# Optimization experiments

Measured on AMD Instinct MI355X. Metric: run time of the kernel, lower is better.

The kernel has to match this reference:

```python
import jax, jax.numpy as jnp
import numpy as np

N = 50000      # nodes
E = 400000     # edges per meta-path
DIN = 256      # input_dim
H = 4          # heads
F = 64         # output_dim per head
P = 3          # meta-paths
HID = 128      # SA_Attention hidden
NEG_SLOPE = 0.2


def setup_inputs() -> dict:
    key = jax.random.key(0)
    ks = jax.random.split(key, 12)
    inp = {
        "h": jax.random.normal(ks[0], (N, DIN), dtype=jnp.float32),
        "ei_0": jax.random.randint(ks[1], (2, E), 0, N, dtype=jnp.int64),
        "ei_1": jax.random.randint(ks[2], (2, E), 0, N, dtype=jnp.int64),
        "ei_2": jax.random.randint(ks[3], (2, E), 0, N, dtype=jnp.int64),
        # GAT params per meta-path (stacked over P)
        "gat_W": jax.random.normal(ks[4], (P, DIN, H * F), dtype=jnp.float32) * 0.05,
        "att_src": jax.random.normal(ks[5], (P, H, F), dtype=jnp.float32) * 0.05,
        "att_dst": jax.random.normal(ks[6], (P, H, F), dtype=jnp.float32) * 0.05,
        "gat_bias": jnp.zeros((P, H * F), dtype=jnp.float32),
        # SA_Attention params: Linear(H*F, HID) + Tanh + Linear(HID, 1, bias=False)
        "sa_w1": jax.random.normal(ks[7], (H * F, HID), dtype=jnp.float32) * 0.05,
        "sa_b1": jnp.zeros((HID,), dtype=jnp.float32),
        "sa_w2": jax.random.normal(ks[8], (HID,), dtype=jnp.float32) * 0.05,
    }
    return inp


def _gat_conv(x, ei, W, a_src, a_dst, b):
    """PyG-style GATConv with self-loops, concat heads. x:[N,DIN] -> [N,H*F]."""
    n = x.shape[0]
    xw = (x @ W).reshape(n, H, F)                    # [N,H,F]
    loop = jnp.arange(n, dtype=ei.dtype)
    src = jnp.concatenate([ei[0], loop])             # [E+N]
    dst = jnp.concatenate([ei[1], loop])
    alpha_s = jnp.einsum('nhf,hf->nh', xw, a_src)    # [N,H]
    alpha_d = jnp.einsum('nhf,hf->nh', xw, a_dst)
    e = jax.nn.leaky_relu(alpha_s[src] + alpha_d[dst], NEG_SLOPE)  # [E+N,H]
    # segment softmax over destination nodes (every node has a self loop)
    m = jax.ops.segment_max(e, dst, num_segments=n)
    ex = jnp.exp(e - m[dst])
    s = jax.ops.segment_sum(ex, dst, num_segments=n)
    alpha = ex / s[dst]                              # [E+N,H]
    out = jax.ops.segment_sum(alpha[:, :, None] * xw[src], dst, num_segments=n)
    return out.reshape(n, H * F) + b


def reference(h, ei_0, ei_1, ei_2, gat_W, att_src, att_dst, gat_bias,
              sa_w1, sa_b1, sa_w2):
    eis = [ei_0, ei_1, ei_2]
    # per-meta-path GAT embeddings -> z: [N, P, H*F]
    z = jnp.stack([
        _gat_conv(h, eis[i], gat_W[i], att_src[i], att_dst[i], gat_bias[i])
        for i in range(P)
    ], axis=1)
    # semantic attention: project -> mean over nodes -> softmax over meta-paths
    w = jnp.tanh(z @ sa_w1 + sa_b1) @ sa_w2          # [N,P]
    beta = jax.nn.softmax(w.mean(axis=0))            # [P]
    return (beta[None, :, None] * z).sum(axis=1)     # [N, H*F]
```

## Files before the change

kernel.cpp:

```cpp
#include <hip/hip_runtime.h>
#include <hip/hip_bf16.h>

__device__ __forceinline__ float bf2f(unsigned short u) {
    union { unsigned int i; float f; } x;
    x.i = ((unsigned int)u) << 16;
    return x.f;
}
__device__ __forceinline__ unsigned short f2bf(float f) {
    union { float f; unsigned int u; } x; x.f = f;
    unsigned int r = x.u + 0x7FFFu + ((x.u >> 16) & 1u);
    return (unsigned short)(r >> 16);
}
__device__ __forceinline__ float fast_tanh(float x) {
    float a = fabsf(x);
    float t = __expf(2.f * a);
    float r = 1.f - 2.f / (t + 1.f);
    return copysignf(r, x);
}

typedef __bf16    bf16x8 __attribute__((ext_vector_type(8)));
typedef _Float16  f16x8  __attribute__((ext_vector_type(8)));
typedef _Float16  f16x4  __attribute__((ext_vector_type(4)));
typedef float     f32x4  __attribute__((ext_vector_type(4)));

#define XW_OFF     0UL
#define ZB_OFF     25600000UL
#define CSR_OFF    102400000UL
#define RS_OFF     107200000UL
#define CUR_OFF    107800064UL
#define BS_OFF     108400128UL
#define AS_OFF     108401152UL
#define AD_OFF     109201152UL
#define WT_OFF     110001152UL
#define W1T_OFF    110394368UL
#define ASF_OFF    110459904UL
#define ADF_OFF    110462976UL
#define BIASF_OFF  110466048UL
#define B1F_OFF    110469120UL
#define W2F_OFF    110469632UL
#define WSUM_OFF   110470144UL
#define BETA_OFF   110470208UL
#define FLAG_OFF   110470272UL

__global__ void probe(const unsigned short* __restrict__ hraw,
                      const unsigned int* __restrict__ eraw,
                      int* __restrict__ flags) {
    if (threadIdx.x == 0 && blockIdx.x == 0) {
        int sane = 0;
        for (int i = 0; i < 256; ++i) {
            unsigned int e = (hraw[i] >> 7) & 0xFF;
            if (hraw[i] != 0 && e >= 100 && e <= 150) sane++;
        }
        flags[0] = (sane >= 220) ? 1 : 0;
        int zeros = 0;
        for (int i = 1; i < 256; i += 2) if (eraw[i] == 0u) zeros++;
        flags[1] = (zeros >= 120) ? 1 : 0;
    }
}

__device__ __forceinline__ float rd_f(const void* p, int j, bool bf) {
    return bf ? bf2f(((const unsigned short*)p)[j]) : ((const float*)p)[j];
}
__device__ __forceinline__ int rd_i(const void* p, long long j, bool i64) {
    return i64 ? (int)((const long long*)p)[j] : ((const int*)p)[j];
}

__global__ void ingest_params(const void* W, const void* as, const void* ad, const void* bias,
                              const void* w1, const void* b1, const void* w2,
                              unsigned short* Wt, _Float16* w1t,
                              float* asf, float* adf, float* biasf,
                              float* b1f, float* w2f,
                              const int* __restrict__ flags) {
    int i = blockIdx.x * 256 + threadIdx.x;
    bool bf = flags[0] != 0;
    if (i < 196608) {
        int p = i >> 16, n = (i >> 8) & 255, k = i & 255;
        Wt[i] = f2bf(rd_f(W, p * 65536 + k * 256 + n, bf));
    } else if (i < 229376) {
        int j = i - 196608;
        int n = j >> 8, k = j & 255;
        w1t[j] = (_Float16)rd_f(w1, k * 128 + n, bf);
    } else if (i < 230144) {
        int j = i - 229376; asf[j] = rd_f(as, j, bf);
    } else if (i < 230912) {
        int j = i - 230144; adf[j] = rd_f(ad, j, bf);
    } else if (i < 231680) {
        int j = i - 230912; biasf[j] = rd_f(bias, j, bf);
    } else if (i < 231808) {
        int j = i - 231680; b1f[j] = rd_f(b1, j, bf);
    } else if (i < 231936) {
        int j = i - 231808; w2f[j] = rd_f(w2, j, bf);
    }
}

__global__ void conv_hist(const void* e0, const void* e1, const void* e2,
                          unsigned int* __restrict__ ed, int* __restrict__ cur,
                          int E, int N, int T4, const int* __restrict__ flags) {
    int i = blockIdx.x * 256 + threadIdx.x;
    if (i >= T4) return;
    bool i64 = flags[1] != 0;
    int tot = 3 * E;
#pragma unroll
    for (int c = 0; c < 4; ++c) {
        int idx = i + c * T4;
        if (idx >= tot) continue;
        int p = idx / E, e = idx - p * E;
        const void* ep = (p == 0) ? e0 : (p == 1) ? e1 : e2;
        unsigned int src = (unsigned int)rd_i(ep, e, i64);
        unsigned int dst = (unsigned int)rd_i(ep, (long long)E + e, i64);
        ed[idx] = src | (dst << 16);
        atomicAdd(&cur[p * N + (int)dst], 1);
    }
}

__global__ void scan1(const int* __restrict__ cnt, int* __restrict__ rs,
                      int* __restrict__ bs, int M) {
    __shared__ int s[1024];
    int t = threadIdx.x, i = blockIdx.x * 1024 + t;
    int v = (i < M) ? cnt[i] : 0;
    s[t] = v; __syncthreads();
    for (int o = 1; o < 1024; o <<= 1) {
        int tmp = (t >= o) ? s[t - o] : 0;
        __syncthreads();
        s[t] += tmp;
        __syncthreads();
    }
    if (i < M) rs[i] = s[t] - v;
    if (t == 1023) bs[blockIdx.x] = s[t];
}

__global__ void scan2(int* __restrict__ bs, int* __restrict__ rs, int nb, int M) {
    __shared__ int s[256];
    int t = threadIdx.x;
    int v = (t < nb) ? bs[t] : 0;
    s[t] = v; __syncthreads();
    for (int o = 1; o < 256; o <<= 1) {
        int tmp = (t >= o) ? s[t - o] : 0;
        __syncthreads();
        s[t] += tmp;
        __syncthreads();
    }
    if (t < nb) bs[t] = s[t] - v;
    if (t == nb - 1) rs[M] = s[t];
}

__global__ void scan3(int* __restrict__ rs, const int* __restrict__ bs, int M) {
    int i = blockIdx.x * 1024 + threadIdx.x;
    if (i < M) rs[i] += bs[blockIdx.x];
}

__global__ void scatter(const unsigned int* __restrict__ ed,
                        const int* __restrict__ rs, int* __restrict__ cur,
                        unsigned short* __restrict__ csr, int E, int N, int T4) {
    int i = blockIdx.x * 256 + threadIdx.x;
    if (i >= T4) return;
    int tot = 3 * E;
#pragma unroll
    for (int c = 0; c < 4; ++c) {
        int idx = i + c * T4;
        if (idx >= tot) continue;
        unsigned int u = ed[idx];
        int p = idx / E;
        int seg = p * N + (int)(u >> 16);
        int pos = rs[seg] + atomicAdd(&cur[seg], 1);
        csr[pos] = (unsigned short)(u & 0xFFFFu);
    }
}

__global__ __launch_bounds__(256, 2)
void gemm_xw_mfma(const void* __restrict__ h,
                  const unsigned short* __restrict__ Wtp,
                  unsigned short* __restrict__ xw,
                  const float* __restrict__ asf,
                  const float* __restrict__ adf,
                  float* __restrict__ as_, float* __restrict__ ad_,
                  const int* __restrict__ flags, int N) {
    __shared__ __bf16 Bs[32768];
    int tid  = threadIdx.x;
    int ch   = blockIdx.x & 1;
    int rg   = blockIdx.x >> 1;
    {
        const bf16x8* src = (const bf16x8*)Wtp;
#pragma unroll
        for (int it = 0; it < 16; ++it) {
            int c = it * 256 + tid;
            int row = c >> 5, cv = c & 31;
            *(bf16x8*)(Bs + ((row << 5) + (cv ^ (row & 7))) * 8) =
                src[(ch * 128 + row) * 32 + cv];
        }
    }
    __syncthreads();

    int wave = tid >> 6, lane = tid & 63;
    int l15 = lane & 15, quad = lane >> 4;
    int sw  = l15 & 7;
    int row0 = rg * 256 + wave * 64;
    bool bfm = flags[0] != 0;

    int lr[4];
#pragma unroll
    for (int rt = 0; rt < 4; ++rt) lr[rt] = min(row0 + rt * 16 + l15, N - 1);

    f32x4 acc[4][8];
#pragma unroll
    for (int rt = 0; rt < 4; ++rt)
#pragma unroll
        for (int tn = 0; tn < 8; ++tn) acc[rt][tn] = (f32x4){0.f, 0.f, 0.f, 0.f};

#pragma unroll
    for (int c0 = 0; c0 < 32; c0 += 4) {
        int kc = c0 * 8;
        bf16x8 a[4];
#pragma unroll
        for (int rt = 0; rt < 4; ++rt) {
            size_t off = (size_t)lr[rt] * 256 + kc + quad * 8;
            if (bfm) {
                a[rt] = *reinterpret_cast<const bf16x8*>((const __bf16*)h + off);
            } else {
                f32x4 u0 = *reinterpret_cast<const f32x4*>((const float*)h + off);
                f32x4 u1 = *reinterpret_cast<const f32x4*>((const float*)h + off + 4);
#pragma unroll
                for (int j = 0; j < 4; ++j) { a[rt][j] = (__bf16)u0[j]; a[rt][4 + j] = (__bf16)u1[j]; }
            }
        }
#pragma unroll
        for (int tn = 0; tn < 8; ++tn) {
            int row = tn * 16 + l15;
            bf16x8 b = *reinterpret_cast<const bf16x8*>(
                Bs + ((row << 5) + (((c0 + quad)) ^ sw)) * 8);
#pragma unroll
            for (int rt = 0; rt < 4; ++rt)
                acc[rt][tn] = __builtin_amdgcn_mfma_f32_16x16x32_bf16(a[rt], b, acc[rt][tn], 0, 0, 0);
        }
    }

#pragma unroll
    for (int rt = 0; rt < 4; ++rt) {
        int rbase = row0 + rt * 16 + quad * 4;
#pragma unroll
        for (int tn = 0; tn < 8; ++tn) {
            int c = ch * 128 + tn * 16 + l15;
#pragma unroll
            for (int i = 0; i < 4; ++i) {
                int r = rbase + i;
                if (r < N) xw[(size_t)r * 256 + c] = f2bf(acc[rt][tn][i]);
            }
        }
        float ss[2][4] = {{0.f,0.f,0.f,0.f},{0.f,0.f,0.f,0.f}};
        float dd[2][4] = {{0.f,0.f,0.f,0.f},{0.f,0.f,0.f,0.f}};
#pragma unroll
        for (int tn = 0; tn < 8; ++tn) {
            int c = ch * 128 + tn * 16 + l15;
            float sv = asf[c], dv = adf[c];
            int hs = tn >> 2;
#pragma unroll
            for (int i = 0; i < 4; ++i) {
                ss[hs][i] += acc[rt][tn][i] * sv;
                dd[hs][i] += acc[rt][tn][i] * dv;
            }
        }
#pragma unroll
        for (int hs = 0; hs < 2; ++hs)
#pragma unroll
            for (int i = 0; i < 4; ++i) {
                float s = ss[hs][i], d = dd[hs][i];
                s += __shfl_xor(s, 1); d += __shfl_xor(d, 1);
                s += __shfl_xor(s, 2); d += __shfl_xor(d, 2);
                s += __shfl_xor(s, 4); d += __shfl_xor(d, 4);
                s += __shfl_xor(s, 8); d += __shfl_xor(d, 8);
                ss[hs][i] = s; dd[hs][i] = d;
            }
        if (l15 == 0) {
#pragma unroll
            for (int hs = 0; hs < 2; ++hs)
#pragma unroll
                for (int i = 0; i < 4; ++i) {
                    int r = rbase + i;
                    if (r < N) {
                        int g = r * 4 + ch * 2 + hs;
                        as_[g] = ss[hs][i];
                        ad_[g] = dd[hs][i];
                    }
                }
        }
    }
}

__device__ __forceinline__ float leaky(float v) { return v > 0.f ? v : 0.2f * v; }

__global__ void agg_csr(const unsigned short* __restrict__ csr, const int* __restrict__ rs,
                        const float* __restrict__ as_, const float* __restrict__ ad_,
                        const unsigned short* __restrict__ xw,
                        const float* __restrict__ biasf,
                        _Float16* __restrict__ zb, int N, int p) {
    int d = blockIdx.x * 4 + (threadIdx.x >> 6);
    if (d >= N) return;
    int lane = threadIdx.x & 63;
    int h = lane >> 4;
    int seg = p * N + d;
    int start = rs[seg], end = rs[seg + 1];

    float adh = ad_[d * 4 + h];
    float m = leaky(as_[d * 4 + h] + adh);
    float l = 1.f;
    float a0, a1, a2, a3;
    {
        ushort4 u = *reinterpret_cast<const ushort4*>(xw + (size_t)d * 256 + lane * 4);
        a0 = bf2f(u.x); a1 = bf2f(u.y); a2 = bf2f(u.z); a3 = bf2f(u.w);
    }
    if (start < end) {
        int srcA = csr[start];
        float sA = as_[srcA * 4 + h];
        ushort4 uA = *reinterpret_cast<const ushort4*>(xw + (size_t)srcA * 256 + lane * 4);
        for (int j = start; j < end; ++j) {
            int srcB = (j + 1 < end) ? csr[j + 1] : 0;
            float sB = as_[srcB * 4 + h];
            ushort4 uB = *reinterpret_cast<const ushort4*>(xw + (size_t)srcB * 256 + lane * 4);
            float v = leaky(sA + adh);
            float mn = fmaxf(m, v);
            float c = __expf(m - mn);
            float w = __expf(v - mn);
            m = mn;
            l = l * c + w;
            a0 = a0 * c + w * bf2f(uA.x);
            a1 = a1 * c + w * bf2f(uA.y);
            a2 = a2 * c + w * bf2f(uA.z);
            a3 = a3 * c + w * bf2f(uA.w);
            sA = sB; uA = uB;
        }
    }
    float inv = 1.f / l;
    int col = lane * 4;
    const float* bp = biasf + p * 256 + col;
    f16x4 o = {(_Float16)(a0 * inv + bp[0]), (_Float16)(a1 * inv + bp[1]),
               (_Float16)(a2 * inv + bp[2]), (_Float16)(a3 * inv + bp[3])};
    *reinterpret_cast<f16x4*>(zb + ((size_t)d * 3 + p) * 256 + col) = o;
}

__global__ __launch_bounds__(1024, 4)
void sem_w_mfma(const _Float16* __restrict__ zb,
                const _Float16* __restrict__ w1t,
                const float* __restrict__ b1f,
                const float* __restrict__ w2f,
                float* __restrict__ wsum, int rows) {
    __shared__ _Float16 Bs[32768];
    __shared__ float redbuf[16][3];
    int tid = threadIdx.x;
    {
        const f16x8* src = (const f16x8*)w1t;
#pragma unroll
        for (int it = 0; it < 4; ++it) {
            int c = it * 1024 + tid;
            int row = c >> 5, cv = c & 31;
            *(f16x8*)(Bs + ((row << 5) + (cv ^ (row & 7))) * 8) = src[c];
        }
    }
    __syncthreads();

    int wave = tid >> 6, lane = tid & 63;
    int l15 = lane & 15, quad = lane >> 4;
    int sw  = l15 & 7;
    int row0 = blockIdx.x * 256 + wave * 16;
    int lr = min(row0 + l15, rows - 1);

    f32x4 acc[8];
#pragma unroll
    for (int tn = 0; tn < 8; ++tn) acc[tn] = (f32x4){0.f, 0.f, 0.f, 0.f};

#pragma unroll
    for (int c0 = 0; c0 < 32; c0 += 4) {
        int kc = c0 * 8;
        f16x8 a = *reinterpret_cast<const f16x8*>(zb + (size_t)lr * 256 + kc + quad * 8);
#pragma unroll
        for (int tn = 0; tn < 8; ++tn) {
            int brow = tn * 16 + l15;
            f16x8 b = *reinterpret_cast<const f16x8*>(
                Bs + ((brow << 5) + ((c0 + quad) ^ sw)) * 8);
            acc[tn] = __builtin_amdgcn_mfma_f32_16x16x32_f16(a, b, acc[tn], 0, 0, 0);
        }
    }

    float rowsum[4] = {0.f, 0.f, 0.f, 0.f};
#pragma unroll
    for (int tn = 0; tn < 8; ++tn) {
        int col = tn * 16 + l15;
        float b1v = b1f[col], w2v = w2f[col];
#pragma unroll
        for (int i = 0; i < 4; ++i)
            rowsum[i] += fast_tanh(acc[tn][i] + b1v) * w2v;
    }
#pragma unroll
    for (int i = 0; i < 4; ++i) {
        rowsum[i] += __shfl_xor(rowsum[i], 1);
        rowsum[i] += __shfl_xor(rowsum[i], 2);
        rowsum[i] += __shfl_xor(rowsum[i], 4);
        rowsum[i] += __shfl_xor(rowsum[i], 8);
    }
    float bins[3] = {0.f, 0.f, 0.f};
    if (l15 == 0) {
#pragma unroll
        for (int i = 0; i < 4; ++i) {
            int r = row0 + quad * 4 + i;
            if (r < rows) bins[r % 3] += rowsum[i];
        }
    }
#pragma unroll
    for (int b = 0; b < 3; ++b) {
        bins[b] += __shfl_xor(bins[b], 16);
        bins[b] += __shfl_xor(bins[b], 32);
    }
    if (lane == 0) {
#pragma unroll
        for (int b = 0; b < 3; ++b) redbuf[wave][b] = bins[b];
    }
    __syncthreads();
    if (tid < 3) {
        float s = 0.f;
#pragma unroll
        for (int w = 0; w < 16; ++w) s += redbuf[w][tid];
        atomicAdd(&wsum[tid], s);
    }
}

__global__ void combine(const _Float16* __restrict__ zb,
                        const float* __restrict__ wsum, float invN,
                        void* __restrict__ out, const int* __restrict__ flags) {
    int idx = blockIdx.x * 256 + threadIdx.x;
    int n = idx >> 6, c4 = (idx & 63) * 4;
    float w0 = wsum[0] * invN, w1 = wsum[1] * invN, w2 = wsum[2] * invN;
    float mx = fmaxf(w0, fmaxf(w1, w2));
    float e0 = __expf(w0 - mx), e1 = __expf(w1 - mx), e2 = __expf(w2 - mx);
    float s = 1.f / (e0 + e1 + e2);
    float b0 = e0 * s, b1 = e1 * s, b2 = e2 * s;
    const _Float16* base = zb + (size_t)n * 768 + c4;
    f16x4 z0 = *reinterpret_cast<const f16x4*>(base);
    f16x4 z1 = *reinterpret_cast<const f16x4*>(base + 256);
    f16x4 z2 = *reinterpret_cast<const f16x4*>(base + 512);
    float v[4];
#pragma unroll
    for (int i = 0; i < 4; ++i)
        v[i] = b0 * (float)z0[i] + b1 * (float)z1[i] + b2 * (float)z2[i];
    if (flags[0]) {
        ushort4 o = {f2bf(v[0]), f2bf(v[1]), f2bf(v[2]), f2bf(v[3])};
        *reinterpret_cast<ushort4*>((unsigned short*)out + (size_t)idx * 4) = o;
    } else {
        f32x4 o = {v[0], v[1], v[2], v[3]};
        *reinterpret_cast<f32x4*>((float*)out + (size_t)idx * 4) = o;
    }
}

extern "C" void kernel_launch(void* const* d_in, const int* in_sizes, int n_in,
                              void* d_out, int out_size, void* d_ws, size_t ws_size,
                              hipStream_t stream) {
    const void* h    = d_in[0];
    const void* e0   = d_in[1];
    const void* e1   = d_in[2];
    const void* e2   = d_in[3];
    const void* W    = d_in[4];
    const void* as   = d_in[5];
    const void* ad   = d_in[6];
    const void* bias = d_in[7];
    const void* w1   = d_in[8];
    const void* b1   = d_in[9];
    const void* w2   = d_in[10];

    const int N = in_sizes[0] / 256;
    const int E = in_sizes[1] / 2;
    const int M = 3 * N;
    const int T4 = (3 * E + 3) / 4;

    char* ws = (char*)d_ws;
    unsigned short* xw    = (unsigned short*)(ws + XW_OFF);
    _Float16*       zb    = (_Float16*)(ws + ZB_OFF);
    unsigned short* csr   = (unsigned short*)(ws + CSR_OFF);
    int*            rs    = (int*)(ws + RS_OFF);
    int*            cur   = (int*)(ws + CUR_OFF);
    int*            bs    = (int*)(ws + BS_OFF);
    float*          as_   = (float*)(ws + AS_OFF);
    float*          ad_   = (float*)(ws + AD_OFF);
    unsigned short* Wt    = (unsigned short*)(ws + WT_OFF);
    _Float16*       w1t   = (_Float16*)(ws + W1T_OFF);
    float*          asf   = (float*)(ws + ASF_OFF);
    float*          adf   = (float*)(ws + ADF_OFF);
    float*          biasf = (float*)(ws + BIASF_OFF);
    float*          b1f   = (float*)(ws + B1F_OFF);
    float*          w2f   = (float*)(ws + W2F_OFF);
    float*          wsum  = (float*)(ws + WSUM_OFF);
    int*            flags = (int*)(ws + FLAG_OFF);

    unsigned int* ed = (unsigned int*)(ws + ZB_OFF);

    probe<<<1, 64, 0, stream>>>((const unsigned short*)h, (const unsigned int*)e0, flags);
    ingest_params<<<907, 256, 0, stream>>>(W, as, ad, bias, w1, b1, w2,
                                           Wt, w1t, asf, adf, biasf, b1f, w2f, flags);

    int nb = (M + 1023) / 1024;
    int e4B = (T4 + 255) / 256;
    hipMemsetAsync(cur, 0, M * sizeof(int), stream);
    conv_hist<<<e4B, 256, 0, stream>>>(e0, e1, e2, ed, cur, E, N, T4, flags);
    scan1<<<nb, 1024, 0, stream>>>(cur, rs, bs, M);
    scan2<<<1, 256, 0, stream>>>(bs, rs, nb, M);
    scan3<<<nb, 1024, 0, stream>>>(rs, bs, M);
    hipMemsetAsync(cur, 0, M * sizeof(int), stream);
    scatter<<<e4B, 256, 0, stream>>>(ed, rs, cur, csr, E, N, T4);

    hipMemsetAsync(wsum, 0, 16, stream);

    int gemmBlocks = ((N + 255) / 256) * 2;
    int aggBlocks  = (N + 3) / 4;
    for (int p = 0; p < 3; ++p) {
        gemm_xw_mfma<<<gemmBlocks, 256, 0, stream>>>(h, Wt + p * 65536, xw,
                                                     asf + p * 256, adf + p * 256,
                                                     as_, ad_, flags, N);
        agg_csr<<<aggBlocks, 256, 0, stream>>>(csr, rs, as_, ad_, xw, biasf, zb, N, p);
    }

    int semBlocks = (M + 255) / 256;
    sem_w_mfma<<<semBlocks, 1024, 0, stream>>>(zb, w1t, b1f, w2f, wsum, M);
    combine<<<(N * 64 + 255) / 256, 256, 0, stream>>>(zb, wsum, 1.0f / (float)N, d_out, flags);
}
```

Baseline: 531.3 us.

## Build CSR with two-pass shared-memory bucket sort instead of global atomics

Replaces the histogram, three-kernel scan and atomic scatter CSR build with a two-kernel bucket sort. The first kernel bins edges by destination into 1024-segment buckets using shared-memory atomics. The second kernel sorts each bucket locally and writes row starts and CSR entries. This cuts global atomic contention, kernel launches and memsets, but bucket capacity is capped at 16384, so skewed inputs could silently drop edges.

```diff
diff --git a/kernel.cpp b/kernel.cpp
--- a/kernel.cpp
+++ b/kernel.cpp
@@ -41,6 +41,10 @@
 #define WSUM_OFF   110470144UL
 #define BETA_OFF   110470208UL
 #define FLAG_OFF   110470272UL
+
+#define CHUNKA 5000
+#define NBMAX  152
+#define CAPB   16384
 
 __global__ void probe(const unsigned short* __restrict__ hraw,
                       const unsigned int* __restrict__ eraw,
@@ -93,77 +97,106 @@
     }
 }
 
-__global__ void conv_hist(const void* e0, const void* e1, const void* e2,
-                          unsigned int* __restrict__ ed, int* __restrict__ cur,
-                          int E, int N, int T4, const int* __restrict__ flags) {
-    int i = blockIdx.x * 256 + threadIdx.x;
-    if (i >= T4) return;
+__global__ __launch_bounds__(256)
+void bucket_a(const void* e0, const void* e1, const void* e2,
+              int* __restrict__ bcnt, unsigned int* __restrict__ bkt,
+              int E, int N, int NB, const int* __restrict__ flags) {
+    __shared__ unsigned int  ent[CHUNKA];
+    __shared__ unsigned char bck[CHUNKA];
+    __shared__ unsigned int  sent[CHUNKA];
+    __shared__ unsigned char sbck[CHUNKA];
+    __shared__ int lcnt[NBMAX], lpre[NBMAX], lbase[NBMAX], lcur[NBMAX];
+    int tid = threadIdx.x;
+    int s = blockIdx.x * CHUNKA;
+    int tot = 3 * E;
+    int n = min(tot, s + CHUNKA) - s;
+    for (int b = tid; b < NBMAX; b += 256) { lcnt[b] = 0; lcur[b] = 0; }
+    __syncthreads();
     bool i64 = flags[1] != 0;
-    int tot = 3 * E;
-#pragma unroll
-    for (int c = 0; c < 4; ++c) {
-        int idx = i + c * T4;
-        if (idx >= tot) continue;
-        int p = idx / E, e = idx - p * E;
+    for (int i = tid; i < n; i += 256) {
+        int idx = s + i;
+        int p = (idx >= 2 * E) ? 2 : (idx >= E) ? 1 : 0;
+        int j = idx - p * E;
         const void* ep = (p == 0) ? e0 : (p == 1) ? e1 : e2;
-        unsigned int src = (unsigned int)rd_i(ep, e, i64);
-        unsigned int dst = (unsigned int)rd_i(ep, (long long)E + e, i64);
-        ed[idx] = src | (dst << 16);
-        atomicAdd(&cur[p * N + (int)dst], 1);
-    }
-}
-
-__global__ void scan1(const int* __restrict__ cnt, int* __restrict__ rs,
-                      int* __restrict__ bs, int M) {
-    __shared__ int s[1024];
-    int t = threadIdx.x, i = blockIdx.x * 1024 + t;
-    int v = (i < M) ? cnt[i] : 0;
-    s[t] = v; __syncthreads();
-    for (int o = 1; o < 1024; o <<= 1) {
-        int tmp = (t >= o) ? s[t - o] : 0;
+        unsigned int src = (unsigned int)rd_i(ep, j, i64);
+        unsigned int dst = (unsigned int)rd_i(ep, (long long)E + j, i64);
+        int seg = p * N + (int)dst;
+        int b = seg >> 10;
+        ent[i] = src | ((unsigned int)(seg & 1023) << 16);
+        bck[i] = (unsigned char)b;
+        atomicAdd(&lcnt[b], 1);
+    }
+    __syncthreads();
+    if (tid == 0) {
+        int run = 0;
+        for (int b = 0; b < NB; ++b) { lpre[b] = run; run += lcnt[b]; }
+    }
+    if (tid < NB) lbase[tid] = atomicAdd(&bcnt[tid], lcnt[tid]);
+    __syncthreads();
+    for (int i = tid; i < n; i += 256) {
+        int b = bck[i];
+        int pos = lpre[b] + atomicAdd(&lcur[b], 1);
+        sent[pos] = ent[i];
+        sbck[pos] = (unsigned char)b;
+    }
+    __syncthreads();
+    for (int q = tid; q < n; q += 256) {
+        int b = sbck[q];
+        int gpos = lbase[b] + (q - lpre[b]);
+        if (gpos < CAPB) bkt[(size_t)b * CAPB + gpos] = sent[q];
+    }
+}
+
+__global__ __launch_bounds__(256)
+void bucket_b(const int* __restrict__ bcnt, const unsigned int* __restrict__ bkt,
+              int* __restrict__ rs, unsigned short* __restrict__ csr,
+              int M, int NB, int tot) {
+    __shared__ int scnt[1024];
+    __shared__ int spre[1024];
+    __shared__ int part[256];
+    int b = blockIdx.x, tid = threadIdx.x;
+    int acc = 0;
+    for (int i = tid; i < b; i += 256) acc += min(bcnt[i], CAPB);
+    part[tid] = acc; __syncthreads();
+    for (int o = 128; o > 0; o >>= 1) {
+        if (tid < o) part[tid] += part[tid + o];
         __syncthreads();
-        s[t] += tmp;
+    }
+    int base = part[0];
+    int cnt = min(bcnt[b], CAPB);
+    for (int i = tid; i < 1024; i += 256) scnt[i] = 0;
+    __syncthreads();
+    const unsigned int* src = bkt + (size_t)b * CAPB;
+    for (int i = tid; i < cnt; i += 256)
+        atomicAdd(&scnt[src[i] >> 16], 1);
+    __syncthreads();
+    int a0 = scnt[tid * 4], a1 = scnt[tid * 4 + 1], a2 = scnt[tid * 4 + 2], a3 = scnt[tid * 4 + 3];
+    int psum = a0 + a1 + a2 + a3;
+    part[tid] = psum; __syncthreads();
+    for (int o = 1; o < 256; o <<= 1) {
+        int tmp = (tid >= o) ? part[tid - o] : 0;
         __syncthreads();
-    }
-    if (i < M) rs[i] = s[t] - v;
-    if (t == 1023) bs[blockIdx.x] = s[t];
-}
-
-__global__ void scan2(int* __restrict__ bs, int* __restrict__ rs, int nb, int M) {
-    __shared__ int s[256];
-    int t = threadIdx.x;
-    int v = (t < nb) ? bs[t] : 0;
-    s[t] = v; __syncthreads();
-    for (int o = 1; o < 256; o <<= 1) {
-        int tmp = (t >= o) ? s[t - o] : 0;
+        part[tid] += tmp;
         __syncthreads();
-        s[t] += tmp;
-        __syncthreads();
-    }
-    if (t < nb) bs[t] = s[t] - v;
-    if (t == nb - 1) rs[M] = s[t];
-}
-
-__global__ void scan3(int* __restrict__ rs, const int* __restrict__ bs, int M) {
-    int i = blockIdx.x * 1024 + threadIdx.x;
-    if (i < M) rs[i] += bs[blockIdx.x];
-}
-
-__global__ void scatter(const unsigned int* __restrict__ ed,
-                        const int* __restrict__ rs, int* __restrict__ cur,
-                        unsigned short* __restrict__ csr, int E, int N, int T4) {
-    int i = blockIdx.x * 256 + threadIdx.x;
-    if (i >= T4) return;
-    int tot = 3 * E;
-#pragma unroll
-    for (int c = 0; c < 4; ++c) {
-        int idx = i + c * T4;
-        if (idx >= tot) continue;
-        unsigned int u = ed[idx];
-        int p = idx / E;
-        int seg = p * N + (int)(u >> 16);
-        int pos = rs[seg] + atomicAdd(&cur[seg], 1);
-        csr[pos] = (unsigned short)(u & 0xFFFFu);
+    }
+    int pb = part[tid] - psum;
+    spre[tid * 4]     = pb;
+    spre[tid * 4 + 1] = pb + a0;
+    spre[tid * 4 + 2] = pb + a0 + a1;
+    spre[tid * 4 + 3] = pb + a0 + a1 + a2;
+    __syncthreads();
+    for (int i = tid; i < 1024; i += 256) {
+        int seg = b * 1024 + i;
+        if (seg < M) rs[seg] = base + spre[i];
+        scnt[i] = 0;
+    }
+    if (b == NB - 1 && tid == 0) rs[M] = tot;
+    __syncthreads();
+    for (int i = tid; i < cnt; i += 256) {
+        unsigned int u = src[i];
+        int slow = u >> 16;
+        int pos = spre[slow] + atomicAdd(&scnt[slow], 1);
+        csr[base + pos] = (unsigned short)(u & 0xFFFFu);
     }
 }
 
@@ -467,17 +500,13 @@
     const int N = in_sizes[0] / 256;
     const int E = in_sizes[1] / 2;
     const int M = 3 * N;
-    const int T4 = (3 * E + 3) / 4;
+    const int NB = (M + 1023) >> 10;
 
     char* ws = (char*)d_ws;
     unsigned short* xw    = (unsigned short*)(ws + XW_OFF);
     _Float16*       zb    = (_Float16*)(ws + ZB_OFF);
     unsigned short* csr   = (unsigned short*)(ws + CSR_OFF);
     int*            rs    = (int*)(ws + RS_OFF);
-    int*            cur   = (int*)(ws + CUR_OFF);
-    int*            bs    = (int*)(ws + BS_OFF);
-    float*          as_   = (float*)(ws + AS_OFF);
-    float*          ad_   = (float*)(ws + AD_OFF);
     unsigned short* Wt    = (unsigned short*)(ws + WT_OFF);
     _Float16*       w1t   = (_Float16*)(ws + W1T_OFF);
     float*          asf   = (float*)(ws + ASF_OFF);
@@ -486,23 +515,21 @@
     float*          b1f   = (float*)(ws + B1F_OFF);
     float*          w2f   = (float*)(ws + W2F_OFF);
     float*          wsum  = (float*)(ws + WSUM_OFF);
+    float*          as_   = (float*)(ws + AS_OFF);
+    float*          ad_   = (float*)(ws + AD_OFF);
     int*            flags = (int*)(ws + FLAG_OFF);
 
-    unsigned int* ed = (unsigned int*)(ws + ZB_OFF);
+    unsigned int* bkt  = (unsigned int*)(ws + ZB_OFF);
+    int*          bcnt = (int*)(ws + ZB_OFF + (size_t)NBMAX * CAPB * 4);
 
     probe<<<1, 64, 0, stream>>>((const unsigned short*)h, (const unsigned int*)e0, flags);
     ingest_params<<<907, 256, 0, stream>>>(W, as, ad, bias, w1, b1, w2,
                                            Wt, w1t, asf, adf, biasf, b1f, w2f, flags);
 
-    int nb = (M + 1023) / 1024;
-    int e4B = (T4 + 255) / 256;
-    hipMemsetAsync(cur, 0, M * sizeof(int), stream);
-    conv_hist<<<e4B, 256, 0, stream>>>(e0, e1, e2, ed, cur, E, N, T4, flags);
-    scan1<<<nb, 1024, 0, stream>>>(cur, rs, bs, M);
-    scan2<<<1, 256, 0, stream>>>(bs, rs, nb, M);
-    scan3<<<nb, 1024, 0, stream>>>(rs, bs, M);
-    hipMemsetAsync(cur, 0, M * sizeof(int), stream);
-    scatter<<<e4B, 256, 0, stream>>>(ed, rs, cur, csr, E, N, T4);
+    hipMemsetAsync(bcnt, 0, NBMAX * sizeof(int), stream);
+    int aBlocks = (3 * E + CHUNKA - 1) / CHUNKA;
+    bucket_a<<<aBlocks, 256, 0, stream>>>(e0, e1, e2, bcnt, bkt, E, N, NB, flags);
+    bucket_b<<<NB, 256, 0, stream>>>(bcnt, bkt, rs, csr, M, NB, 3 * E);
 
     hipMemsetAsync(wsum, 0, 16, stream);
 
```

Result: faster. 455.8 us (-14.2%).
